# Kernel tuning notes

Hardware: AMD Instinct MI355X
Metric: run time of the kernel (lower is better)

The kernel has to match this reference:

```python
import jax, jax.numpy as jnp
import numpy as np

N_NODES = 10000
N_EDGES = 160000
F_IN = 50          # PPI num_features
H = 4              # attention heads
C_BODY = 256       # body GAT out channels per head -> concat 1024
C_HEAD = 64        # head GAT out channels per head -> concat 256
T = 121            # PPI num_classes (one task head each)
D_BODY = H * C_BODY   # 1024
D_HEAD = H * C_HEAD   # 256


def setup_inputs() -> dict:
    key = jax.random.key(0)
    ks = jax.random.split(key, 18)
    inv = lambda f: 1.0 / np.sqrt(f)
    x = jax.random.normal(ks[0], (N_NODES, F_IN), dtype=jnp.float32)
    edge_index = jax.random.randint(ks[1], (2, N_EDGES), 0, N_NODES, dtype=jnp.int64)
    # body GATConv(50 -> 256, heads=4)
    W_body = jax.random.normal(ks[2], (F_IN, H, C_BODY), jnp.float32) * inv(F_IN)
    a_src_body = jax.random.normal(ks[3], (H, C_BODY), jnp.float32) * 0.1
    a_dst_body = jax.random.normal(ks[4], (H, C_BODY), jnp.float32) * 0.1
    b_body = jnp.zeros((D_BODY,), jnp.float32)
    # body Linear(50 -> 1024)
    Wfc_body = jax.random.normal(ks[5], (F_IN, D_BODY), jnp.float32) * inv(F_IN)
    bfc_body = jnp.zeros((D_BODY,), jnp.float32)
    # stacked per-task head GATConv(1024 -> 64, heads=4)
    Wh = jax.random.normal(ks[6], (T, D_BODY, H, C_HEAD), jnp.float32) * inv(D_BODY)
    a_src_h = jax.random.normal(ks[7], (T, H, C_HEAD), jnp.float32) * 0.1
    a_dst_h = jax.random.normal(ks[8], (T, H, C_HEAD), jnp.float32) * 0.1
    b_h = jnp.zeros((T, D_HEAD), jnp.float32)
    # stacked per-task Linear(1024 -> 256)
    W1 = jax.random.normal(ks[9], (T, D_BODY, D_HEAD), jnp.float32) * inv(D_BODY)
    b1 = jnp.zeros((T, D_HEAD), jnp.float32)
    # stacked per-task Linear(256 -> 2)
    W2 = jax.random.normal(ks[10], (T, D_HEAD, 2), jnp.float32) * inv(D_HEAD)
    b2 = jnp.zeros((T, 2), jnp.float32)
    return dict(x=x, edge_index=edge_index,
                W_body=W_body, a_src_body=a_src_body, a_dst_body=a_dst_body, b_body=b_body,
                Wfc_body=Wfc_body, bfc_body=bfc_body,
                Wh=Wh, a_src_h=a_src_h, a_dst_h=a_dst_h, b_h=b_h,
                W1=W1, b1=b1, W2=W2, b2=b2)


def gat_conv(x, W, a_src, a_dst, bias, src, dst, num_nodes):
    """PyG GATConv (concat=True, negative_slope=0.2). src/dst include self loops."""
    h = jnp.einsum('nf,fhc->nhc', x, W)                      # [N,H,C]
    al_src = jnp.sum(h * a_src, axis=-1)                     # [N,H]
    al_dst = jnp.sum(h * a_dst, axis=-1)                     # [N,H]
    e = jax.nn.leaky_relu(al_src[src] + al_dst[dst], 0.2)    # [E,H]
    # segment softmax over incoming edges of each target node
    m = jax.lax.stop_gradient(jax.ops.segment_max(e, dst, num_segments=num_nodes))
    ex = jnp.exp(e - m[dst])
    denom = jax.ops.segment_sum(ex, dst, num_segments=num_nodes)
    alpha = ex / (denom[dst] + 1e-16)                        # [E,H]
    out = jax.ops.segment_sum(alpha[:, :, None] * h[src], dst, num_segments=num_nodes)
    return out.reshape(num_nodes, -1) + bias                 # [N,H*C]


def reference(x, edge_index, W_body, a_src_body, a_dst_body, b_body,
              Wfc_body, bfc_body, Wh, a_src_h, a_dst_h, b_h, W1, b1, W2, b2):
    n = x.shape[0]
    loops = jnp.arange(n, dtype=edge_index.dtype)
    src = jnp.concatenate([edge_index[0], loops])   # add_self_loops=True
    dst = jnp.concatenate([edge_index[1], loops])
    x1 = jax.nn.elu(gat_conv(x, W_body, a_src_body, a_dst_body, b_body, src, dst, n)
                    + x @ Wfc_body + bfc_body)      # [N,1024]

    def head(params):
        Wh_t, as_t, ad_t, bh_t, W1_t, b1_t, W2_t, b2_t = params
        xh = jax.nn.elu(gat_conv(x1, Wh_t, as_t, ad_t, bh_t, src, dst, n)
                        + x1 @ W1_t + b1_t)         # [N,256]
        return xh @ W2_t + b2_t                     # [N,2]

    out = jax.lax.map(head, (Wh, a_src_h, a_dst_h, b_h, W1, b1, W2, b2))
    return out  # [T, N, 2], stacked version of the original list of 121 outputs
```

## Files before the change

kernel.cpp:

```cpp
#include <hip/hip_runtime.h>

typedef unsigned short u16;
typedef unsigned int u32;
typedef __attribute__((ext_vector_type(8))) short short8;
typedef __attribute__((ext_vector_type(4))) float f32x4;

#define NN 10000
#define NE 160000
#define ET 170000
#define FI 50
#define DB 1024
#define NT 121

static __device__ __forceinline__ float bf2f(u16 b) { return __uint_as_float(((u32)b) << 16); }
static __device__ __forceinline__ u16 f2bf(float f) {
  u32 u = __float_as_uint(f);
  u += 0x7FFFu + ((u >> 16) & 1u);
  return (u16)(u >> 16);
}
static __device__ __forceinline__ float eluf(float x) { return x > 0.f ? x : __expf(x) - 1.f; }
static __device__ __forceinline__ float lrelu(float x) { return x > 0.f ? x : 0.2f * x; }

__device__ __forceinline__ void gload16(const void* g, void* l) {
  __builtin_amdgcn_global_load_lds((const __attribute__((address_space(1))) u32*)g,
                                   (__attribute__((address_space(3))) u32*)l, 16, 0, 0);
}

__global__ __launch_bounds__(256) void k_detect(const int* __restrict__ ei, int* flag) {
  int any = 0;
  for (int i = threadIdx.x; i < NE; i += 256) any |= ei[2 * i + 1];
  if (any) flag[0] = 1;
}

__global__ __launch_bounds__(256) void k_deg(const int* __restrict__ ei, const int* __restrict__ flag,
                                             int* deg) {
  int e = blockIdx.x * 256 + threadIdx.x;
  if (e >= ET) return;
  int is32 = flag[0];
  int d = (e < NE) ? (is32 ? ei[NE + e] : ei[2 * (NE + e)]) : (e - NE);
  atomicAdd(&deg[d], 1);
}

__global__ __launch_bounds__(256) void k_scan(const int* __restrict__ deg, int* __restrict__ rowptr) {
  __shared__ int ps[256];
  int tid = threadIdx.x;
  int s = 0;
  for (int i = 0; i < 40; i++) { int idx = tid * 40 + i; if (idx < NN) s += deg[idx]; }
  ps[tid] = s;
  __syncthreads();
  if (tid == 0) {
    int run = 0;
    for (int i = 0; i < 256; i++) { int v = ps[i]; ps[i] = run; run += v; }
    rowptr[NN] = run;
  }
  __syncthreads();
  int run = ps[tid];
  for (int i = 0; i < 40; i++) {
    int idx = tid * 40 + i;
    if (idx < NN) { rowptr[idx] = run; run += deg[idx]; }
  }
}

__global__ __launch_bounds__(256) void k_fill(const int* __restrict__ ei, const int* __restrict__ flag,
                                              const int* __restrict__ rowptr, int* fill, int* csr) {
  int e = blockIdx.x * 256 + threadIdx.x;
  if (e >= ET) return;
  int is32 = flag[0];
  int s, d;
  if (e < NE) { s = is32 ? ei[e] : ei[2 * e]; d = is32 ? ei[NE + e] : ei[2 * (NE + e)]; }
  else { s = d = e - NE; }
  int pos = atomicAdd(&fill[d], 1);
  csr[rowptr[d] + pos] = s;
}

__global__ __launch_bounds__(256) void k_body_gemm(const float* __restrict__ x, const float* __restrict__ Wb,
                                                   const float* __restrict__ Wfc,
                                                   u16* __restrict__ h_body, u16* __restrict__ xfc) {
  __shared__ float xs[32][52];
  int tid = threadIdx.x;
  int m0 = blockIdx.x * 32;
  for (int i = tid; i < 32 * FI; i += 256) {
    int r = i / FI, c = i - r * FI;
    int row = m0 + r; if (row > NN - 1) row = NN - 1;
    xs[r][c] = x[(size_t)row * FI + c];
  }
  __syncthreads();
  int col = blockIdx.y * 256 + tid;
  const float* Wp; u16* op;
  if (col < DB) { Wp = Wb + col; op = h_body + col; }
  else { Wp = Wfc + (col - DB); op = xfc + (col - DB); }
  float acc[32];
  #pragma unroll
  for (int m = 0; m < 32; m++) acc[m] = 0.f;
  for (int k = 0; k < FI; k++) {
    float wv = Wp[(size_t)k * DB];
    #pragma unroll
    for (int m = 0; m < 32; m++) acc[m] += xs[m][k] * wv;
  }
  #pragma unroll
  for (int m = 0; m < 32; m++) {
    int row = m0 + m;
    if (row < NN) op[(size_t)row * DB] = f2bf(acc[m]);
  }
}

__global__ __launch_bounds__(64) void k_body_al(const u16* __restrict__ h_body, const float* __restrict__ as,
                                                const float* __restrict__ ad, float* __restrict__ al) {
  int n = blockIdx.x, l = threadIdx.x;
  const u16* hr = h_body + (size_t)n * DB + l * 16;
  const float* ap = as + l * 16;
  const float* dp = ad + l * 16;
  float ss = 0.f, sd = 0.f;
  #pragma unroll
  for (int i = 0; i < 16; i++) { float hv = bf2f(hr[i]); ss += hv * ap[i]; sd += hv * dp[i]; }
  #pragma unroll
  for (int o = 1; o < 16; o <<= 1) { ss += __shfl_xor(ss, o); sd += __shfl_xor(sd, o); }
  if ((l & 15) == 0) { int h = l >> 4; al[(size_t)n * 8 + h] = ss; al[(size_t)n * 8 + 4 + h] = sd; }
}

__global__ __launch_bounds__(256) void k_body_agg(const u16* __restrict__ h_body, const u16* __restrict__ xfc,
                                                  const float* __restrict__ al, const int* __restrict__ rowptr,
                                                  const int* __restrict__ csr, const float* __restrict__ bb,
                                                  const float* __restrict__ bfc, u16* __restrict__ x1b) {
  __shared__ float wl[256];
  __shared__ int sl[64];
  int n = blockIdx.x, tid = threadIdx.x;
  int c0 = tid * 4, h = tid >> 6;
  float acc0 = 0, acc1 = 0, acc2 = 0, acc3 = 0, wsum = 0;
  int beg = rowptr[n], end = rowptr[n + 1];
  for (int base = beg; base < end; base += 64) {
    int cnt = end - base; if (cnt > 64) cnt = 64;
    int slot = tid >> 2, hh = tid & 3;
    if (slot < cnt) {
      int s = csr[base + slot];
      if (hh == 0) sl[slot] = s;
      float e = al[(size_t)s * 8 + hh] + al[(size_t)n * 8 + 4 + hh];
      wl[slot * 4 + hh] = __expf(lrelu(e));
    }
    __syncthreads();
    for (int j = 0; j < cnt; j++) {
      float wv = wl[j * 4 + h];
      int s = sl[j];
      ushort4 hv = *(const ushort4*)(h_body + (size_t)s * DB + c0);
      acc0 += wv * bf2f(hv.x); acc1 += wv * bf2f(hv.y);
      acc2 += wv * bf2f(hv.z); acc3 += wv * bf2f(hv.w);
      wsum += wv;
    }
    __syncthreads();
  }
  float inv = 1.f / (wsum + 1e-16f);
  ushort4 xf = *(const ushort4*)(xfc + (size_t)n * DB + c0);
  ushort4 o;
  o.x = f2bf(eluf(acc0 * inv + bb[c0 + 0] + bf2f(xf.x) + bfc[c0 + 0]));
  o.y = f2bf(eluf(acc1 * inv + bb[c0 + 1] + bf2f(xf.y) + bfc[c0 + 1]));
  o.z = f2bf(eluf(acc2 * inv + bb[c0 + 2] + bf2f(xf.z) + bfc[c0 + 2]));
  o.w = f2bf(eluf(acc3 * inv + bb[c0 + 3] + bf2f(xf.w) + bfc[c0 + 3]));
  *(ushort4*)(x1b + (size_t)n * DB + c0) = o;
}

__global__ __launch_bounds__(256) void k_trans_w(const float* __restrict__ Wh, const float* __restrict__ W1,
                                                 u16* __restrict__ Wt, int t0) {
  __shared__ float tile[64][65];
  int t = t0 + blockIdx.z;
  int k0 = blockIdx.x * 64, n0 = blockIdx.y * 64;
  const float* Wsrc = (n0 < 256) ? (Wh + (size_t)t * 1024 * 256 + n0)
                                 : (W1 + (size_t)t * 1024 * 256 + (n0 - 256));
  int tid = threadIdx.x;
  for (int i = tid; i < 4096; i += 256) {
    int kr = i >> 6, nc = i & 63;
    tile[kr][nc] = Wsrc[(size_t)(k0 + kr) * 256 + nc];
  }
  __syncthreads();
  u16* dst = Wt + ((size_t)blockIdx.z * 512 + n0) * 1024 + k0;
  for (int i = tid; i < 4096; i += 256) {
    int nr = i >> 6, kc = i & 63;
    dst[(size_t)nr * 1024 + kc] = f2bf(tile[kc][nr]);
  }
}

__global__ __launch_bounds__(512, 4) void k_task_gemm(const u16* __restrict__ x1b, const u16* __restrict__ Wt,
                                                      u16* __restrict__ HT, int Gc) {
  __shared__ alignas(16) u16 As[3][4096];
  __shared__ alignas(16) u16 Bs[3][8192];
  int tid = threadIdx.x;
  int sRow = tid >> 2, sQ = tid & 3;
  int sA = (sQ + (sRow >> 1)) & 3;
  int m0 = blockIdx.x * 128;
  int bn = blockIdx.y;
  int r0 = m0 + sRow; if (r0 > NN - 1) r0 = NN - 1;
  const u16* Ag = x1b + (size_t)r0 * 1024 + sA * 8;
  const u16* BgBase = Wt + ((size_t)(bn * 256) + sRow) * 1024 + sA * 8;
  int dstOff = tid * 8;
  int wv = tid >> 6, lane = tid & 63;
  int wm = wv >> 2, wn = wv & 3;
  int q = ((lane >> 4) - ((lane & 15) >> 1)) & 3;
  int fragOff = (lane & 15) * 32 + q * 8;
  int AfO = (wm * 64) * 32 + fragOff;
  int BfO = (wn * 64) * 32 + fragOff;

  int zbeg = blockIdx.z * 2;
  int zend = zbeg + 2; if (zend > Gc) zend = Gc;
  for (int z = zbeg; z < zend; z++) {
    const u16* Bg0 = BgBase + (size_t)z * 524288;
    const u16* Bg1 = Bg0 + 131072;
    f32x4 acc[4][4];
    #pragma unroll
    for (int a = 0; a < 4; a++)
      #pragma unroll
      for (int b = 0; b < 4; b++) acc[a][b] = (f32x4){0.f, 0.f, 0.f, 0.f};

#define STAGE(kt_, slot_)                              \
    do {                                               \
      int _k = (kt_) * 32;                             \
      gload16(Ag + _k, &As[slot_][dstOff]);            \
      gload16(Bg0 + _k, &Bs[slot_][dstOff]);           \
      gload16(Bg1 + _k, &Bs[slot_][4096 + dstOff]);    \
    } while (0)

    STAGE(0, 0);
    STAGE(1, 1);

    #pragma unroll
    for (int kt = 0; kt < 32; kt++) {
      if (kt < 31) asm volatile("s_waitcnt vmcnt(3)" ::: "memory");
      else         asm volatile("s_waitcnt vmcnt(0)" ::: "memory");
      __builtin_amdgcn_s_barrier();
      __builtin_amdgcn_sched_barrier(0);
      int s = kt % 3;
      if (kt + 2 < 32) STAGE(kt + 2, (kt + 2) % 3);
      const u16* Ac = &As[s][0] + AfO;
      const u16* Bc = &Bs[s][0] + BfO;
      short8 af[4], bfr[4];
      #pragma unroll
      for (int a = 0; a < 4; a++) af[a] = *(const short8*)(Ac + a * 512);
      #pragma unroll
      for (int b = 0; b < 4; b++) bfr[b] = *(const short8*)(Bc + b * 512);
      __builtin_amdgcn_s_setprio(1);
      #pragma unroll
      for (int a = 0; a < 4; a++)
        #pragma unroll
        for (int b = 0; b < 4; b++)
          acc[a][b] = __builtin_amdgcn_mfma_f32_16x16x32_bf16(af[a], bfr[b], acc[a][b], 0, 0, 0);
      __builtin_amdgcn_s_setprio(0);
    }
#undef STAGE
    u16* Hb = HT + (size_t)z * NN * 512;
    #pragma unroll
    for (int a = 0; a < 4; a++) {
      int rbase = m0 + wm * 64 + a * 16 + (lane >> 4) * 4;
      #pragma unroll
      for (int b = 0; b < 4; b++) {
        int col = bn * 256 + wn * 64 + b * 16 + (lane & 15);
        #pragma unroll
        for (int r = 0; r < 4; r++) {
          int row = rbase + r;
          if (row < NN) Hb[(size_t)row * 512 + col] = f2bf(acc[a][b][r]);
        }
      }
    }
    __syncthreads();
  }
}

__global__ __launch_bounds__(64) void k_task_al(const u16* __restrict__ HT, const float* __restrict__ ash,
                                                const float* __restrict__ adh, float* __restrict__ ALt, int t0) {
  int n = blockIdx.x, g = blockIdx.y, l = threadIdx.x;
  int t = t0 + g;
  const u16* row = HT + ((size_t)g * NN + n) * 512 + l * 4;
  ushort4 v = *(const ushort4*)row;
  int h = l >> 4, cl = (l * 4) & 63;
  const float* ap = ash + ((size_t)t * 4 + h) * 64 + cl;
  const float* dp = adh + ((size_t)t * 4 + h) * 64 + cl;
  float f0 = bf2f(v.x), f1 = bf2f(v.y), f2 = bf2f(v.z), f3 = bf2f(v.w);
  float ss = f0 * ap[0] + f1 * ap[1] + f2 * ap[2] + f3 * ap[3];
  float sd = f0 * dp[0] + f1 * dp[1] + f2 * dp[2] + f3 * dp[3];
  #pragma unroll
  for (int o = 1; o < 16; o <<= 1) { ss += __shfl_xor(ss, o); sd += __shfl_xor(sd, o); }
  if ((l & 15) == 0) {
    float* dst = ALt + ((size_t)g * NN + n) * 8;
    dst[h] = ss; dst[4 + h] = sd;
  }
}

__global__ __launch_bounds__(64) void k_task_agg_out(const u16* __restrict__ HT, const float* __restrict__ ALt,
                                                     const int* __restrict__ rowptr, const int* __restrict__ csr,
                                                     const float* __restrict__ bh, const float* __restrict__ b1,
                                                     const float* __restrict__ W2, const float* __restrict__ b2,
                                                     float* __restrict__ out, int t0) {
  __shared__ float wl[256];
  __shared__ int sl[64];
  int n = blockIdx.x, g = blockIdx.y, l = threadIdx.x;
  int t = t0 + g;
  int c0 = l * 4, h = l >> 4;
  const u16* Hb = HT + (size_t)g * NN * 512;
  const float* ALg = ALt + (size_t)g * NN * 8;
  float ad0 = ALg[(size_t)n * 8 + 4], ad1 = ALg[(size_t)n * 8 + 5];
  float ad2 = ALg[(size_t)n * 8 + 6], ad3 = ALg[(size_t)n * 8 + 7];
  float acc0 = 0, acc1 = 0, acc2 = 0, acc3 = 0, wsum = 0;
  int beg = rowptr[n], end = rowptr[n + 1];
  for (int base = beg; base < end; base += 64) {
    int cnt = end - base; if (cnt > 64) cnt = 64;
    if (l < cnt) {
      int s = csr[base + l];
      sl[l] = s;
      const float* alsp = ALg + (size_t)s * 8;
      wl[l * 4 + 0] = __expf(lrelu(alsp[0] + ad0));
      wl[l * 4 + 1] = __expf(lrelu(alsp[1] + ad1));
      wl[l * 4 + 2] = __expf(lrelu(alsp[2] + ad2));
      wl[l * 4 + 3] = __expf(lrelu(alsp[3] + ad3));
    }
    __syncthreads();
    for (int j = 0; j < cnt; j++) {
      float wv = wl[j * 4 + h];
      int s = sl[j];
      ushort4 hv = *(const ushort4*)(Hb + (size_t)s * 512 + c0);
      acc0 += wv * bf2f(hv.x); acc1 += wv * bf2f(hv.y);
      acc2 += wv * bf2f(hv.z); acc3 += wv * bf2f(hv.w);
      wsum += wv;
    }
    __syncthreads();
  }
  float inv = 1.f / (wsum + 1e-16f);
  ushort4 fc = *(const ushort4*)(Hb + (size_t)n * 512 + 256 + c0);
  const float* bhp = bh + (size_t)t * 256 + c0;
  const float* b1p = b1 + (size_t)t * 256 + c0;
  const float* w2p = W2 + ((size_t)t * 256 + c0) * 2;
  float o0 = 0, o1 = 0, xv;
  xv = eluf(acc0 * inv + bhp[0] + bf2f(fc.x) + b1p[0]); o0 += xv * w2p[0]; o1 += xv * w2p[1];
  xv = eluf(acc1 * inv + bhp[1] + bf2f(fc.y) + b1p[1]); o0 += xv * w2p[2]; o1 += xv * w2p[3];
  xv = eluf(acc2 * inv + bhp[2] + bf2f(fc.z) + b1p[2]); o0 += xv * w2p[4]; o1 += xv * w2p[5];
  xv = eluf(acc3 * inv + bhp[3] + bf2f(fc.w) + b1p[3]); o0 += xv * w2p[6]; o1 += xv * w2p[7];
  #pragma unroll
  for (int o = 1; o < 64; o <<= 1) { o0 += __shfl_xor(o0, o); o1 += __shfl_xor(o1, o); }
  if (l == 0) {
    float* op = out + ((size_t)t * NN + n) * 2;
    op[0] = o0 + b2[t * 2];
    op[1] = o1 + b2[t * 2 + 1];
  }
}

extern "C" void kernel_launch(void* const* d_in, const int* in_sizes, int n_in,
                              void* d_out, int out_size, void* d_ws, size_t ws_size,
                              hipStream_t stream) {
  const float* x   = (const float*)d_in[0];
  const int*   ei  = (const int*)  d_in[1];
  const float* Wb  = (const float*)d_in[2];
  const float* asb = (const float*)d_in[3];
  const float* adb = (const float*)d_in[4];
  const float* bb  = (const float*)d_in[5];
  const float* Wfc = (const float*)d_in[6];
  const float* bfc = (const float*)d_in[7];
  const float* Wh  = (const float*)d_in[8];
  const float* ash = (const float*)d_in[9];
  const float* adh = (const float*)d_in[10];
  const float* bh  = (const float*)d_in[11];
  const float* W1  = (const float*)d_in[12];
  const float* b1  = (const float*)d_in[13];
  const float* W2  = (const float*)d_in[14];
  const float* b2  = (const float*)d_in[15];
  float* out = (float*)d_out;

  char* w = (char*)d_ws;
  size_t off = 0;
  auto take = [&](size_t b) { size_t o = off; off = (off + b + 255) & ~(size_t)255; return o; };
  u16*   x1b    = (u16*)  (w + take((size_t)NN * DB * 2));
  float* albody = (float*)(w + take((size_t)NN * 8 * 4));
  int*   flag   = (int*)  (w + take(4 + NN * 4 + NN * 4));
  int*   deg    = flag + 1;
  int*   fill   = deg + NN;
  int*   rowptr = (int*)  (w + take((NN + 1) * 4));
  int*   csr    = (int*)  (w + take((size_t)ET * 4));
  size_t Rbase = off;
  u16* h_body = (u16*)(w + Rbase);
  u16* xfc    = h_body + (size_t)NN * DB;
  const size_t perTask = 1048576 + 10240000 + 320000;
  size_t avail = ws_size > Rbase ? ws_size - Rbase : 0;
  int G = (int)(avail / perTask);
  if (G < 1) G = 1;
  if (G > NT) G = NT;
  u16*   Wt  = (u16*)(w + Rbase);
  u16*   HT  = Wt + (size_t)G * 524288;
  float* ALt = (float*)(HT + (size_t)G * 5120000);

  hipMemsetAsync(flag, 0, 4 + NN * 4 + NN * 4, stream);
  k_detect<<<1, 256, 0, stream>>>(ei, flag);
  k_deg<<<(ET + 255) / 256, 256, 0, stream>>>(ei, flag, deg);
  k_scan<<<1, 256, 0, stream>>>(deg, rowptr);
  k_fill<<<(ET + 255) / 256, 256, 0, stream>>>(ei, flag, rowptr, fill, csr);
  k_body_gemm<<<dim3(313, 8), 256, 0, stream>>>(x, Wb, Wfc, h_body, xfc);
  k_body_al<<<NN, 64, 0, stream>>>(h_body, asb, adb, albody);
  k_body_agg<<<NN, 256, 0, stream>>>(h_body, xfc, albody, rowptr, csr, bb, bfc, x1b);

  for (int t0 = 0; t0 < NT; t0 += G) {
    int Gc = NT - t0; if (Gc > G) Gc = G;
    k_trans_w<<<dim3(16, 8, Gc), 256, 0, stream>>>(Wh, W1, Wt, t0);
    k_task_gemm<<<dim3(79, 2, (Gc + 1) / 2), 512, 0, stream>>>(x1b, Wt, HT, Gc);
    k_task_al<<<dim3(NN, Gc), 64, 0, stream>>>(HT, ash, adh, ALt, t0);
    k_task_agg_out<<<dim3(NN, Gc), 64, 0, stream>>>(HT, ALt, rowptr, csr, bh, b1, W2, b2, out, t0);
  }
}
```

Measured before the change: 3.868 ms.

## Retile task GEMM to 128x128 with XCD-aware block mapping and register prefetch

Shrinks the task GEMM block from 512 threads with a 128x256 tile to 256 threads with a 128x128 tile. Blocks are launched on a flat grid and remapped so consecutive job IDs land on the same XCD, aiming for better L2 reuse of shared A/B tiles. The loop now keeps three global loads in flight and double-buffers LDS fragments in registers so the reads for the next step overlap the current MFMAs. The trade-off is that each block reuses less data per tile, issues more global load traffic overall, and the hand-set waitcnt scheduling is harder to get right.

New measurement: 5.151 ms. 33.2% more time.

```diff
diff --git a/kernel.cpp b/kernel.cpp
--- a/kernel.cpp
+++ b/kernel.cpp
@@ -178,70 +178,105 @@
   }
 }
 
-__global__ __launch_bounds__(512, 4) void k_task_gemm(const u16* __restrict__ x1b, const u16* __restrict__ Wt,
-                                                      u16* __restrict__ HT, int Gc) {
+__global__ __launch_bounds__(256) void k_task_gemm(const u16* __restrict__ x1b, const u16* __restrict__ Wt,
+                                                   u16* __restrict__ HT, int Gc, int q) {
   __shared__ alignas(16) u16 As[3][4096];
-  __shared__ alignas(16) u16 Bs[3][8192];
+  __shared__ alignas(16) u16 Bs[3][4096];
+  int zp = (Gc + 1) / 2;
+  int jid = (blockIdx.x & 7) * q + (blockIdx.x >> 3);
+  if (jid >= 316 * zp) return;
+  int zpair = jid / 316;
+  int rj = jid - zpair * 316;
+  int bm = rj >> 2, bn = rj & 3;
   int tid = threadIdx.x;
   int sRow = tid >> 2, sQ = tid & 3;
   int sA = (sQ + (sRow >> 1)) & 3;
-  int m0 = blockIdx.x * 128;
-  int bn = blockIdx.y;
-  int r0 = m0 + sRow; if (r0 > NN - 1) r0 = NN - 1;
-  const u16* Ag = x1b + (size_t)r0 * 1024 + sA * 8;
-  const u16* BgBase = Wt + ((size_t)(bn * 256) + sRow) * 1024 + sA * 8;
-  int dstOff = tid * 8;
+  int m0 = bm * 128;
+  int r0 = m0 + sRow;      if (r0 > NN - 1) r0 = NN - 1;
+  int r1 = m0 + 64 + sRow; if (r1 > NN - 1) r1 = NN - 1;
+  const u16* Ag0 = x1b + (size_t)r0 * 1024 + sA * 8;
+  const u16* Ag1 = x1b + (size_t)r1 * 1024 + sA * 8;
+  const u16* Bg0base = Wt + ((size_t)(bn * 128) + sRow) * 1024 + sA * 8;
+  const u16* Bg1base = Bg0base + (size_t)64 * 1024;
   int wv = tid >> 6, lane = tid & 63;
-  int wm = wv >> 2, wn = wv & 3;
-  int q = ((lane >> 4) - ((lane & 15) >> 1)) & 3;
-  int fragOff = (lane & 15) * 32 + q * 8;
+  int wm = wv >> 1, wn = wv & 1;
+  int qr = ((lane >> 4) - ((lane & 15) >> 1)) & 3;
+  int fragOff = (lane & 15) * 32 + qr * 8;
   int AfO = (wm * 64) * 32 + fragOff;
   int BfO = (wn * 64) * 32 + fragOff;
 
-  int zbeg = blockIdx.z * 2;
+  int zbeg = zpair * 2;
   int zend = zbeg + 2; if (zend > Gc) zend = Gc;
   for (int z = zbeg; z < zend; z++) {
-    const u16* Bg0 = BgBase + (size_t)z * 524288;
-    const u16* Bg1 = Bg0 + 131072;
+    const u16* Bg0 = Bg0base + (size_t)z * 524288;
+    const u16* Bg1 = Bg1base + (size_t)z * 524288;
     f32x4 acc[4][4];
     #pragma unroll
     for (int a = 0; a < 4; a++)
       #pragma unroll
       for (int b = 0; b < 4; b++) acc[a][b] = (f32x4){0.f, 0.f, 0.f, 0.f};
 
-#define STAGE(kt_, slot_)                              \
-    do {                                               \
-      int _k = (kt_) * 32;                             \
-      gload16(Ag + _k, &As[slot_][dstOff]);            \
-      gload16(Bg0 + _k, &Bs[slot_][dstOff]);           \
-      gload16(Bg1 + _k, &Bs[slot_][4096 + dstOff]);    \
+#define STAGE(kt_, slot_)                               \
+    do {                                                \
+      int _k = (kt_) * 32;                              \
+      gload16(Ag0 + _k, &As[slot_][tid * 8]);           \
+      gload16(Ag1 + _k, &As[slot_][2048 + tid * 8]);    \
+      gload16(Bg0 + _k, &Bs[slot_][tid * 8]);           \
+      gload16(Bg1 + _k, &Bs[slot_][2048 + tid * 8]);    \
     } while (0)
 
     STAGE(0, 0);
     STAGE(1, 1);
-
+    STAGE(2, 2);
+    asm volatile("s_waitcnt vmcnt(8)" ::: "memory");
+    __builtin_amdgcn_s_barrier();
+    __builtin_amdgcn_sched_barrier(0);
+    short8 afA[4], bfA[4], afB[4], bfB[4];
     #pragma unroll
+    for (int a = 0; a < 4; a++) afA[a] = *(const short8*)(&As[0][0] + AfO + a * 512);
+    #pragma unroll
+    for (int b = 0; b < 4; b++) bfA[b] = *(const short8*)(&Bs[0][0] + BfO + b * 512);
+
+    int scur = 0, snxt = 1;
+    #pragma unroll 2
     for (int kt = 0; kt < 32; kt++) {
-      if (kt < 31) asm volatile("s_waitcnt vmcnt(3)" ::: "memory");
+      if (kt < 30) asm volatile("s_waitcnt vmcnt(4)" ::: "memory");
       else         asm volatile("s_waitcnt vmcnt(0)" ::: "memory");
+      asm volatile("s_waitcnt lgkmcnt(0)" ::: "memory");
       __builtin_amdgcn_s_barrier();
       __builtin_amdgcn_sched_barrier(0);
-      int s = kt % 3;
-      if (kt + 2 < 32) STAGE(kt + 2, (kt + 2) % 3);
-      const u16* Ac = &As[s][0] + AfO;
-      const u16* Bc = &Bs[s][0] + BfO;
-      short8 af[4], bfr[4];
-      #pragma unroll
-      for (int a = 0; a < 4; a++) af[a] = *(const short8*)(Ac + a * 512);
-      #pragma unroll
-      for (int b = 0; b < 4; b++) bfr[b] = *(const short8*)(Bc + b * 512);
-      __builtin_amdgcn_s_setprio(1);
-      #pragma unroll
-      for (int a = 0; a < 4; a++)
+      if (kt < 29) STAGE(kt + 3, scur);
+      if ((kt & 1) == 0) {
+        if (kt < 31) {
+          #pragma unroll
+          for (int a = 0; a < 4; a++) afB[a] = *(const short8*)(&As[snxt][0] + AfO + a * 512);
+          #pragma unroll
+          for (int b = 0; b < 4; b++) bfB[b] = *(const short8*)(&Bs[snxt][0] + BfO + b * 512);
+        }
+        __builtin_amdgcn_s_setprio(1);
         #pragma unroll
-        for (int b = 0; b < 4; b++)
-          acc[a][b] = __builtin_amdgcn_mfma_f32_16x16x32_bf16(af[a], bfr[b], acc[a][b], 0, 0, 0);
-      __builtin_amdgcn_s_setprio(0);
+        for (int a = 0; a < 4; a++)
+          #pragma unroll
+          for (int b = 0; b < 4; b++)
+            acc[a][b] = __builtin_amdgcn_mfma_f32_16x16x32_bf16(afA[a], bfA[b], acc[a][b], 0, 0, 0);
+        __builtin_amdgcn_s_setprio(0);
+      } else {
+        if (kt < 31) {
+          #pragma unroll
+          for (int a = 0; a < 4; a++) afA[a] = *(const short8*)(&As[snxt][0] + AfO + a * 512);
+          #pragma unroll
+          for (int b = 0; b < 4; b++) bfA[b] = *(const short8*)(&Bs[snxt][0] + BfO + b * 512);
+        }
+        __builtin_amdgcn_s_setprio(1);
+        #pragma unroll
+        for (int a = 0; a < 4; a++)
+          #pragma unroll
+          for (int b = 0; b < 4; b++)
+            acc[a][b] = __builtin_amdgcn_mfma_f32_16x16x32_bf16(afB[a], bfB[b], acc[a][b], 0, 0, 0);
+        __builtin_amdgcn_s_setprio(0);
+      }
+      int t1 = scur + 1; scur = (t1 == 3) ? 0 : t1;
+      int t2 = snxt + 1; snxt = (t2 == 3) ? 0 : t2;
     }
 #undef STAGE
     u16* Hb = HT + (size_t)z * NN * 512;
@@ -250,7 +285,7 @@
       int rbase = m0 + wm * 64 + a * 16 + (lane >> 4) * 4;
       #pragma unroll
       for (int b = 0; b < 4; b++) {
-        int col = bn * 256 + wn * 64 + b * 16 + (lane & 15);
+        int col = bn * 128 + wn * 64 + b * 16 + (lane & 15);
         #pragma unroll
         for (int r = 0; r < 4; r++) {
           int row = rbase + r;
@@ -393,8 +428,11 @@
 
   for (int t0 = 0; t0 < NT; t0 += G) {
     int Gc = NT - t0; if (Gc > G) Gc = G;
+    int zp = (Gc + 1) / 2;
+    int jobs = 316 * zp;
+    int q = (jobs + 7) / 8;
     k_trans_w<<<dim3(16, 8, Gc), 256, 0, stream>>>(Wh, W1, Wt, t0);
-    k_task_gemm<<<dim3(79, 2, (Gc + 1) / 2), 512, 0, stream>>>(x1b, Wt, HT, Gc);
+    k_task_gemm<<<8 * q, 256, 0, stream>>>(x1b, Wt, HT, Gc, q);
     k_task_al<<<dim3(NN, Gc), 64, 0, stream>>>(HT, ash, adh, ALt, t0);
     k_task_agg_out<<<dim3(NN, Gc), 64, 0, stream>>>(HT, ALt, rowptr, csr, bh, b1, W2, b2, out, t0);
   }
```

## Remap task GEMM blocks XCD-aware and restructure LDS pipeline barrier placement

Applied to the files above, without the earlier changes.

The 3D grid of the task GEMM becomes a 1D grid whose block index is remapped so consecutive jobs land on the same XCD (blockIdx & 7 chooses a chunk), aiming for better L2 reuse of shared A/B tiles. The k-loop is also reordered. Fragments are read from LDS first, then the next stage is issued, and a single wait-plus-barrier follows before the MFMAs. This puts one barrier per iteration after the fragment reads and turns the loop into a rolled one with rotating slot indices. The rolled loop may cost some scheduling quality, and the extra lgkmcnt wait could serialize LDS reads against the MFMAs.

New measurement: 3.285 ms (median of 3 runs). 15.1% less time.

```diff
diff --git a/kernel.cpp b/kernel.cpp
--- a/kernel.cpp
+++ b/kernel.cpp
@@ -179,26 +179,30 @@
 }
 
 __global__ __launch_bounds__(512, 4) void k_task_gemm(const u16* __restrict__ x1b, const u16* __restrict__ Wt,
-                                                      u16* __restrict__ HT, int Gc) {
+                                                      u16* __restrict__ HT, int Gc, int q) {
   __shared__ alignas(16) u16 As[3][4096];
   __shared__ alignas(16) u16 Bs[3][8192];
+  int zp = (Gc + 1) / 2;
+  int jid = (blockIdx.x & 7) * q + (blockIdx.x >> 3);
+  if (jid >= 158 * zp) return;
+  int zpair = jid / 158;
+  int rj = jid - zpair * 158;
+  int bm = rj >> 1, bn = rj & 1;
   int tid = threadIdx.x;
   int sRow = tid >> 2, sQ = tid & 3;
   int sA = (sQ + (sRow >> 1)) & 3;
-  int m0 = blockIdx.x * 128;
-  int bn = blockIdx.y;
+  int m0 = bm * 128;
   int r0 = m0 + sRow; if (r0 > NN - 1) r0 = NN - 1;
   const u16* Ag = x1b + (size_t)r0 * 1024 + sA * 8;
   const u16* BgBase = Wt + ((size_t)(bn * 256) + sRow) * 1024 + sA * 8;
-  int dstOff = tid * 8;
   int wv = tid >> 6, lane = tid & 63;
   int wm = wv >> 2, wn = wv & 3;
-  int q = ((lane >> 4) - ((lane & 15) >> 1)) & 3;
-  int fragOff = (lane & 15) * 32 + q * 8;
+  int qr = ((lane >> 4) - ((lane & 15) >> 1)) & 3;
+  int fragOff = (lane & 15) * 32 + qr * 8;
   int AfO = (wm * 64) * 32 + fragOff;
   int BfO = (wn * 64) * 32 + fragOff;
 
-  int zbeg = blockIdx.z * 2;
+  int zbeg = zpair * 2;
   int zend = zbeg + 2; if (zend > Gc) zend = Gc;
   for (int z = zbeg; z < zend; z++) {
     const u16* Bg0 = BgBase + (size_t)z * 524288;
@@ -212,29 +216,33 @@
 #define STAGE(kt_, slot_)                              \
     do {                                               \
       int _k = (kt_) * 32;                             \
-      gload16(Ag + _k, &As[slot_][dstOff]);            \
-      gload16(Bg0 + _k, &Bs[slot_][dstOff]);           \
-      gload16(Bg1 + _k, &Bs[slot_][4096 + dstOff]);    \
+      gload16(Ag + _k, &As[slot_][tid * 8]);           \
+      gload16(Bg0 + _k, &Bs[slot_][tid * 8]);          \
+      gload16(Bg1 + _k, &Bs[slot_][4096 + tid * 8]);   \
     } while (0)
 
     STAGE(0, 0);
     STAGE(1, 1);
-
-    #pragma unroll
+    asm volatile("s_waitcnt vmcnt(3)" ::: "memory");
+    __builtin_amdgcn_s_barrier();
+    __builtin_amdgcn_sched_barrier(0);
+
+    int scur = 0, stgt = 2;
     for (int kt = 0; kt < 32; kt++) {
-      if (kt < 31) asm volatile("s_waitcnt vmcnt(3)" ::: "memory");
-      else         asm volatile("s_waitcnt vmcnt(0)" ::: "memory");
-      __builtin_amdgcn_s_barrier();
-      __builtin_amdgcn_sched_barrier(0);
-      int s = kt % 3;
-      if (kt + 2 < 32) STAGE(kt + 2, (kt + 2) % 3);
-      const u16* Ac = &As[s][0] + AfO;
-      const u16* Bc = &Bs[s][0] + BfO;
+      const u16* Ac = &As[0][0] + scur * 4096 + AfO;
+      const u16* Bc = &Bs[0][0] + scur * 8192 + BfO;
       short8 af[4], bfr[4];
       #pragma unroll
       for (int a = 0; a < 4; a++) af[a] = *(const short8*)(Ac + a * 512);
       #pragma unroll
       for (int b = 0; b < 4; b++) bfr[b] = *(const short8*)(Bc + b * 512);
+      if (kt + 2 < 32) STAGE(kt + 2, stgt);
+      if (kt < 30) asm volatile("s_waitcnt vmcnt(3)" ::: "memory");
+      else         asm volatile("s_waitcnt vmcnt(0)" ::: "memory");
+      asm volatile("s_waitcnt lgkmcnt(0)" ::: "memory");
+      __builtin_amdgcn_sched_barrier(0);
+      __builtin_amdgcn_s_barrier();
+      __builtin_amdgcn_sched_barrier(0);
       __builtin_amdgcn_s_setprio(1);
       #pragma unroll
       for (int a = 0; a < 4; a++)
@@ -242,6 +250,9 @@
         for (int b = 0; b < 4; b++)
           acc[a][b] = __builtin_amdgcn_mfma_f32_16x16x32_bf16(af[a], bfr[b], acc[a][b], 0, 0, 0);
       __builtin_amdgcn_s_setprio(0);
+      __builtin_amdgcn_sched_barrier(0);
+      int t1 = scur + 1; scur = (t1 == 3) ? 0 : t1;
+      int t2 = stgt + 1; stgt = (t2 == 3) ? 0 : t2;
     }
 #undef STAGE
     u16* Hb = HT + (size_t)z * NN * 512;
@@ -393,8 +404,11 @@
 
   for (int t0 = 0; t0 < NT; t0 += G) {
     int Gc = NT - t0; if (Gc > G) Gc = G;
+    int zp = (Gc + 1) / 2;
+    int jobs = 158 * zp;
+    int q = (jobs + 7) / 8;
     k_trans_w<<<dim3(16, 8, Gc), 256, 0, stream>>>(Wh, W1, Wt, t0);
-    k_task_gemm<<<dim3(79, 2, (Gc + 1) / 2), 512, 0, stream>>>(x1b, Wt, HT, Gc);
+    k_task_gemm<<<8 * q, 512, 0, stream>>>(x1b, Wt, HT, Gc, q);
     k_task_al<<<dim3(NN, Gc), 64, 0, stream>>>(HT, ash, adh, ALt, t0);
     k_task_agg_out<<<dim3(NN, Gc), 64, 0, stream>>>(HT, ALt, rowptr, csr, bh, b1, W2, b2, out, t0);
   }
```
